# Optimization experiments

Hardware: AMD Instinct MI355X
Metric: run time of the kernel (lower is better)

## Reference

```python
import jax, jax.numpy as jnp
import numpy as np

S, B, E, H = 2048, 4, 512, 8
D = E // H

# --- Brevitas-style per-tensor fake quantization with straight-through estimator ---

def fq_s8(x):
    """Int8ActPerTensorFloat / Int8WeightPerTensorFloat: symmetric per-tensor abs-max."""
    qmax = 127.0
    scale = jnp.maximum(jnp.max(jnp.abs(x)), 1e-8) / qmax
    q = jnp.clip(jnp.round(x / scale), -128.0, qmax)
    return x + jax.lax.stop_gradient(scale * q - x), scale


def fq_u8(x):
    """Uint8ActPerTensorFloat for attention weights (softmax output, >=0)."""
    qmax = 255.0
    scale = jnp.maximum(jnp.max(x), 1e-8) / qmax
    q = jnp.clip(jnp.round(x / scale), 0.0, qmax)
    return x + jax.lax.stop_gradient(scale * q - x)


def fq_b32(b, scale):
    """Int32Bias: bias quantized with scale = input_scale * weight_scale."""
    qmax = 2.0 ** 31 - 1.0
    q = jnp.clip(jnp.round(b / scale), -qmax, qmax)
    return b + jax.lax.stop_gradient(scale * q - b)


def setup_inputs() -> dict:
    key = jax.random.key(0)
    ks = jax.random.split(key, 9)
    w = lambda k: jax.random.normal(k, (E, E), jnp.float32) * 0.02
    b = lambda k: jax.random.normal(k, (E,), jnp.float32) * 0.02
    return {
        "x": jax.random.normal(ks[0], (S, B, E), jnp.float32),
        "Wq": w(ks[1]), "Wk": w(ks[2]), "Wv": w(ks[3]),
        "bq": b(ks[4]), "bk": b(ks[5]), "bv": b(ks[6]),
        "Wo": w(ks[7]), "bo": b(ks[8]),
    }


def reference(x, Wq, Wk, Wv, bq, bk, bv, Wo, bo):
    # inputQuant (QuantIdentity, int8)
    xq, _ = fq_s8(x)
    # in_proj input quant (int8, per-tensor)
    xi, s_in = fq_s8(xq)

    def proj(W, b_):
        Wf, s_w = fq_s8(W)                    # int8 weight quant
        bf = fq_b32(b_, s_in * s_w)           # int32 bias quant
        return jnp.einsum('sbe,fe->sbf', xi, Wf) + bf

    q = proj(Wq, bq)  # [S,B,E]
    k = proj(Wk, bk)
    v = proj(Wv, bv)

    # split heads: [S,B,E] -> [B,H,S,D]
    heads = lambda t: t.reshape(S, B, H, D).transpose(1, 2, 0, 3)
    q, k, v = heads(q), heads(k), heads(v)

    qs, _ = fq_s8(q / jnp.sqrt(jnp.float32(D)))   # q_scaled_quant (int8)
    kt, _ = fq_s8(k)                              # k_transposed_quant (int8)
    scores = jnp.einsum('bhqd,bhkd->bhqk', qs, kt)  # [B,H,S,S]
    attn = fq_u8(jax.nn.softmax(scores, axis=-1))   # attn_output_weights_quant (uint8)
    vq, _ = fq_s8(v)                                # v_quant (int8)

    ctx = jnp.einsum('bhqk,bhkd->bhqd', attn, vq)   # [B,H,S,D]
    ctx = ctx.transpose(2, 0, 1, 3).reshape(S, B, E)  # back to [S,B,E]

    ci, s_c = fq_s8(ctx)                            # out_proj_input_quant
    Wof, s_wo = fq_s8(Wo)                           # out_proj_weight_quant
    bof = fq_b32(bo, s_c * s_wo)                    # out_proj_bias_quant
    y = jnp.einsum('sbe,fe->sbf', ci, Wof) + bof
    yq, _ = fq_s8(y)                                # out_proj_output_quant
    return yq
```

## Files before the change

### kernel.cpp

```cpp
#include <hip/hip_runtime.h>

constexpr int cS = 2048, cB = 4, cE = 512, cH = 8, cD = 64;
constexpr int cSB = cS * cB;
constexpr int cBH = cB * cH;
constexpr int cN  = cSB * cE;

typedef __bf16 v8bf  __attribute__((ext_vector_type(8)));
typedef float  f32x4 __attribute__((ext_vector_type(4)));

constexpr float cLOG2E = 1.4426950408889634f;


__device__ __forceinline__ unsigned short q2bf(float f) {
  return (unsigned short)(__float_as_uint(f) >> 16);
}
__device__ __forceinline__ float clip8(float t) { return fminf(fmaxf(t, -128.f), 127.f); }
__device__ __forceinline__ float wave_max(float v) {
#pragma unroll
  for (int o = 32; o > 0; o >>= 1) v = fmaxf(v, __shfl_down(v, o));
  return v;
}

__device__ __forceinline__ void stage8k(const unsigned short* __restrict__ gsrc,
                                        unsigned short* lds, int tid) {
  int w = tid >> 6;
#pragma unroll
  for (int is = 0; is < 2; ++is) {
    int c = is * 256 + tid;
    int cp = (c & ~7) | ((c & 7) ^ ((c >> 3) & 7));
    const char* g = (const char*)gsrc + (size_t)cp * 16;
    char* l = (char*)lds + (size_t)(is * 4096 + w * 1024);
    __builtin_amdgcn_global_load_lds(
        (const __attribute__((address_space(1))) unsigned int*)g,
        (__attribute__((address_space(3))) unsigned int*)l, 16, 0, 0);
  }
}
__device__ __forceinline__ v8bf lds_frag(const unsigned short* tile, int row, int chunk) {
  int sc = chunk ^ (row & 7);
  return *(const v8bf*)((const char*)tile + row * 128 + sc * 16);
}

__global__ void absmax_kernel(const float* __restrict__ p, int n4, unsigned* slot) {
  int tid = blockIdx.x * blockDim.x + threadIdx.x, stride = gridDim.x * blockDim.x;
  float m = 0.f;
  for (int i = tid; i < n4; i += stride) {
    float4 v = ((const float4*)p)[i];
    m = fmaxf(m, fmaxf(fmaxf(fabsf(v.x), fabsf(v.y)), fmaxf(fabsf(v.z), fabsf(v.w))));
  }
  m = wave_max(m);
  __shared__ float sm[4];
  int lane = threadIdx.x & 63, wid = threadIdx.x >> 6;
  if (lane == 0) sm[wid] = m;
  __syncthreads();
  if (threadIdx.x == 0) {
    float mm = sm[0];
    for (int w = 1; w < (int)blockDim.x / 64; ++w) mm = fmaxf(mm, sm[w]);
    atomicMax(slot, __float_as_uint(mm));
  }
}

__global__ void absmax4_kernel(const float* __restrict__ w0, const float* __restrict__ w1,
                               const float* __restrict__ w2, const float* __restrict__ w3,
                               int n4, unsigned* slots) {
  int y = blockIdx.y;
  const float* p = (y == 0) ? w0 : (y == 1) ? w1 : (y == 2) ? w2 : w3;
  int tid = blockIdx.x * blockDim.x + threadIdx.x, stride = gridDim.x * blockDim.x;
  float m = 0.f;
  for (int i = tid; i < n4; i += stride) {
    float4 v = ((const float4*)p)[i];
    m = fmaxf(m, fmaxf(fmaxf(fabsf(v.x), fabsf(v.y)), fmaxf(fabsf(v.z), fabsf(v.w))));
  }
  m = wave_max(m);
  __shared__ float sm[4];
  int lane = threadIdx.x & 63, wid = threadIdx.x >> 6;
  if (lane == 0) sm[wid] = m;
  __syncthreads();
  if (threadIdx.x == 0) {
    float mm = fmaxf(fmaxf(sm[0], sm[1]), fmaxf(sm[2], sm[3]));
    atomicMax(slots + y, __float_as_uint(mm));
  }
}

__global__ void scales_kernel(float* st, int stage) {
  if (stage == 0) {
    float s0 = fmaxf(st[0], 1e-8f) / 127.f;
    st[11] = s0;
    float mxq = s0 * 127.f;
    st[12] = fmaxf(mxq, 1e-8f) / 127.f;
    for (int i = 0; i < 4; ++i) st[13 + i] = fmaxf(st[1 + i], 1e-8f) / 127.f;
  } else if (stage == 1) {
    st[17] = fmaxf(st[5] * 0.125f, 1e-8f) / 127.f;
    st[18] = fmaxf(st[6], 1e-8f) / 127.f;
    st[19] = fmaxf(st[7], 1e-8f) / 127.f;
    st[25] = st[17] * st[18];
    st[26] = st[25] * cLOG2E;
  } else if (stage == 2) {
    float sa = fmaxf(st[8], 1e-8f) / 255.f;
    st[20] = sa; st[21] = 1.f / sa; st[22] = sa * st[19];
  } else if (stage == 3) {
    st[23] = fmaxf(st[9], 1e-8f) / 127.f;
  } else {
    st[24] = fmaxf(st[10], 1e-8f) / 127.f;
  }
}

__global__ void quant_x_kernel(const float* __restrict__ x, unsigned short* __restrict__ xq,
                               const float* st, int n4) {
  float s0 = st[11], si = st[12];
  int tid = blockIdx.x * blockDim.x + threadIdx.x, stride = gridDim.x * blockDim.x;
  for (int i = tid; i < n4; i += stride) {
    float4 v = ((const float4*)x)[i];
    ushort4 o; float t;
    t = s0 * clip8(rintf(v.x / s0)); o.x = q2bf(clip8(rintf(t / si)));
    t = s0 * clip8(rintf(v.y / s0)); o.y = q2bf(clip8(rintf(t / si)));
    t = s0 * clip8(rintf(v.z / s0)); o.z = q2bf(clip8(rintf(t / si)));
    t = s0 * clip8(rintf(v.w / s0)); o.w = q2bf(clip8(rintf(t / si)));
    ((ushort4*)xq)[i] = o;
  }
}

__global__ void quant_w4_kernel(const float* __restrict__ w0, const float* __restrict__ w1,
                                const float* __restrict__ w2, const float* __restrict__ w3,
                                unsigned short* __restrict__ outbase, int n4, const float* st) {
  int y = blockIdx.y;
  const float* in = (y == 0) ? w0 : (y == 1) ? w1 : (y == 2) ? w2 : w3;
  unsigned short* outp = outbase + (size_t)y * cE * cE;
  float s = st[13 + y];
  int tid = blockIdx.x * blockDim.x + threadIdx.x, stride = gridDim.x * blockDim.x;
  for (int i = tid; i < n4; i += stride) {
    float4 v = ((const float4*)in)[i];
    ushort4 o;
    o.x = q2bf(clip8(rintf(v.x / s)));
    o.y = q2bf(clip8(rintf(v.y / s)));
    o.z = q2bf(clip8(rintf(v.z / s)));
    o.w = q2bf(clip8(rintf(v.w / s)));
    ((ushort4*)outp)[i] = o;
  }
}

__global__ void quant_s8_kernel(const float* __restrict__ in, unsigned short* __restrict__ outp,
                                int n4, const float* st, int slot, float premul) {
  float s = st[slot];
  int tid = blockIdx.x * blockDim.x + threadIdx.x, stride = gridDim.x * blockDim.x;
  for (int i = tid; i < n4; i += stride) {
    float4 v = ((const float4*)in)[i];
    ushort4 o;
    o.x = q2bf(clip8(rintf(v.x * premul / s)));
    o.y = q2bf(clip8(rintf(v.y * premul / s)));
    o.z = q2bf(clip8(rintf(v.z * premul / s)));
    o.w = q2bf(clip8(rintf(v.w * premul / s)));
    ((ushort4*)outp)[i] = o;
  }
}

__global__ void quant_qk_kernel(const float* __restrict__ qf, unsigned short* __restrict__ qsb,
                                int n4, const float* st) {
  int y = blockIdx.y;
  const float* in = qf + (size_t)y * cN;
  unsigned short* outp = qsb + (size_t)y * cN;
  float s = st[17 + y];
  float premul = y ? 1.0f : 0.125f;
  int tid = blockIdx.x * blockDim.x + threadIdx.x, stride = gridDim.x * blockDim.x;
  for (int i = tid; i < n4; i += stride) {
    float4 v = ((const float4*)in)[i];
    ushort4 o;
    o.x = q2bf(clip8(rintf(v.x * premul / s)));
    o.y = q2bf(clip8(rintf(v.y * premul / s)));
    o.z = q2bf(clip8(rintf(v.z * premul / s)));
    o.w = q2bf(clip8(rintf(v.w * premul / s)));
    ((ushort4*)outp)[i] = o;
  }
}

__global__ void bias3_kernel(const float* __restrict__ b0, const float* __restrict__ b1,
                             const float* __restrict__ b2, float* __restrict__ bdst,
                             const float* st) {
  int y = blockIdx.y;
  const float* bsrc = (y == 0) ? b0 : (y == 1) ? b1 : b2;
  int f = blockIdx.x * blockDim.x + threadIdx.x;
  if (f < cE) {
    float s = st[12] * st[13 + y];
    bdst[y * cE + f] = s * rintf(bsrc[f] / s);
  }
}

__global__ void bias_kernel(const float* __restrict__ bsrc, float* __restrict__ bdst,
                            const float* st, int slot_in, int slot_w) {
  int f = blockIdx.x * blockDim.x + threadIdx.x;
  if (f < cE) {
    float s = st[slot_in] * st[slot_w];
    bdst[f] = s * rintf(bsrc[f] / s);
  }
}

__global__ __launch_bounds__(256) void quant_vT_kernel(const float* __restrict__ v,
                                                       unsigned short* __restrict__ vT,
                                                       const float* st) {
  __shared__ unsigned short tile[64][65];
  int bh = blockIdx.y, bx = blockIdx.x, s0 = bx * 64;
  float sv = st[19];
  int td = threadIdx.x & 63, tr = threadIdx.x >> 6;
  for (int r = tr; r < 64; r += 4)
    tile[r][td] = q2bf(clip8(rintf(v[((size_t)bh * cS + s0 + r) * cD + td] / sv)));
  __syncthreads();
  for (int r = tr; r < 64; r += 4)
    vT[((size_t)(bh * 32 + bx) * 64 + r) * 64 + td] = tile[td][r];
}

__global__ void final_quant_kernel(float* __restrict__ y, const float* st, int n4) {
  float s = st[24];
  int tid = blockIdx.x * blockDim.x + threadIdx.x, stride = gridDim.x * blockDim.x;
  for (int i = tid; i < n4; i += stride) {
    float4 v = ((float4*)y)[i];
    v.x = s * clip8(rintf(v.x / s)); v.y = s * clip8(rintf(v.y / s));
    v.z = s * clip8(rintf(v.z / s)); v.w = s * clip8(rintf(v.w / s));
    ((float4*)y)[i] = v;
  }
}

template <int OUTMODE>
__global__ __launch_bounds__(256) void gemm_kernel(const unsigned short* __restrict__ A,
                                                   const unsigned short* __restrict__ Wb,
                                                   const float* __restrict__ bias,
                                                   float* __restrict__ out, const float* st,
                                                   int slot_in, int slot_w, unsigned* amax_slot) {
  int wid = threadIdx.x >> 6, lane = threadIdx.x & 63;
  int wm = wid >> 1, wn = wid & 1;
  int row0 = blockIdx.x * 64 + wm * 32;
  int col0 = blockIdx.y * 64 + wn * 32;
  int lr = lane & 15, lk = (lane >> 4) * 8;
  f32x4 acc[2][2] = {};
  const unsigned short* a0p = A + (size_t)(row0 + lr) * cE + lk;
  const unsigned short* a1p = A + (size_t)(row0 + 16 + lr) * cE + lk;
  const unsigned short* b0p = Wb + (size_t)(col0 + lr) * cE + lk;
  const unsigned short* b1p = Wb + (size_t)(col0 + 16 + lr) * cE + lk;
  for (int e0 = 0; e0 < cE; e0 += 32) {
    v8bf a0 = *(const v8bf*)(a0p + e0), a1 = *(const v8bf*)(a1p + e0);
    v8bf b0 = *(const v8bf*)(b0p + e0), b1 = *(const v8bf*)(b1p + e0);
    acc[0][0] = __builtin_amdgcn_mfma_f32_16x16x32_bf16(a0, b0, acc[0][0], 0, 0, 0);
    acc[0][1] = __builtin_amdgcn_mfma_f32_16x16x32_bf16(a0, b1, acc[0][1], 0, 0, 0);
    acc[1][0] = __builtin_amdgcn_mfma_f32_16x16x32_bf16(a1, b0, acc[1][0], 0, 0, 0);
    acc[1][1] = __builtin_amdgcn_mfma_f32_16x16x32_bf16(a1, b1, acc[1][1], 0, 0, 0);
  }
  float scale = st[slot_in] * st[slot_w];
  float lmax = 0.f;
#pragma unroll
  for (int mi = 0; mi < 2; ++mi)
#pragma unroll
    for (int ni = 0; ni < 2; ++ni)
#pragma unroll
      for (int r = 0; r < 4; ++r) {
        int row = row0 + mi * 16 + (lane >> 4) * 4 + r;
        int col = col0 + ni * 16 + lr;
        float val = scale * acc[mi][ni][r] + bias[col];
        lmax = fmaxf(lmax, fabsf(val));
        if (OUTMODE == 0) {
          int s = row >> 2, bb = row & 3, h = col >> 6, d = col & 63;
          out[(((size_t)(bb * cH + h)) * cS + s) * cD + d] = val;
        } else {
          out[(size_t)row * cE + col] = val;
        }
      }
  lmax = wave_max(lmax);
  if (lane == 0) atomicMax(amax_slot, __float_as_uint(lmax));
}

__global__ __launch_bounds__(256) void attn_pass1_kernel(const unsigned short* __restrict__ qs,
                                                         const unsigned short* __restrict__ ks,
                                                         float* __restrict__ marr,
                                                         float* __restrict__ izarr,
                                                         const float* st, unsigned* maxiz_slot) {
  __shared__ __align__(16) unsigned short kbuf[2][64][64];
  int tid = threadIdx.x;
  int bh = blockIdx.y;
  int wid = tid >> 6, lane = tid & 63;
  int lr = lane & 15, g = lane >> 4, lk = g * 8;
  int r0 = blockIdx.x * 64 + wid * 16;
  float sscale2 = st[26];
  v8bf aq0 = *(const v8bf*)(qs + ((size_t)bh * cS + r0 + lr) * cD + lk);
  v8bf aq1 = *(const v8bf*)(qs + ((size_t)bh * cS + r0 + lr) * cD + 32 + lk);
  const unsigned short* Kb = ks + (size_t)bh * cS * cD;

  stage8k(Kb, &kbuf[0][0][0], tid);
  __syncthreads();
  float pm = -1e30f, zs = 0.f;
  int buf = 0;
  for (int t = 0; t < 32; ++t) {
    if (t < 31) stage8k(Kb + (size_t)(t + 1) * 4096, &kbuf[buf ^ 1][0][0], tid);
    const unsigned short* Kt = &kbuf[buf][0][0];
    f32x4 s4[4];
#pragma unroll
    for (int jc = 0; jc < 4; ++jc) {
      v8bf k0 = lds_frag(Kt, jc * 16 + lr, g);
      v8bf k1 = lds_frag(Kt, jc * 16 + lr, g + 4);
      f32x4 z = {0.f, 0.f, 0.f, 0.f};
      z = __builtin_amdgcn_mfma_f32_16x16x32_bf16(k0, aq0, z, 0, 0, 0);
      z = __builtin_amdgcn_mfma_f32_16x16x32_bf16(k1, aq1, z, 0, 0, 0);
      s4[jc] = z;
    }
    float tv[16];
#pragma unroll
    for (int jc = 0; jc < 4; ++jc)
#pragma unroll
      for (int r = 0; r < 4; ++r) tv[jc * 4 + r] = s4[jc][r] * sscale2;
    float tm = tv[0];
#pragma unroll
    for (int i = 1; i < 16; ++i) tm = fmaxf(tm, tv[i]);
    float nm = fmaxf(pm, tm);
    float acc = zs * __builtin_amdgcn_exp2f(pm - nm);
#pragma unroll
    for (int i = 0; i < 16; ++i) acc += __builtin_amdgcn_exp2f(tv[i] - nm);
    zs = acc; pm = nm;
    __syncthreads();
    buf ^= 1;
  }
#pragma unroll
  for (int o = 16; o < 64; o <<= 1) {
    float mo = __shfl_xor(pm, o);
    float zo = __shfl_xor(zs, o);
    float nm = fmaxf(pm, mo);
    zs = zs * __builtin_amdgcn_exp2f(pm - nm) + zo * __builtin_amdgcn_exp2f(mo - nm);
    pm = nm;
  }
  float iz = 1.0f / zs;
  if (g == 0) {
    marr[bh * cS + r0 + lr] = pm;
    izarr[bh * cS + r0 + lr] = iz;
  }
  float wmax = wave_max(iz);
  if (lane == 0) atomicMax(maxiz_slot, __float_as_uint(wmax));
}

__global__ __launch_bounds__(256) void attn_pass2_kernel(
    const unsigned short* __restrict__ qs, const unsigned short* __restrict__ ks,
    const unsigned short* __restrict__ vT, const float* __restrict__ marr,
    const float* __restrict__ izarr, float* __restrict__ ctx, const float* st,
    unsigned* amax_slot) {
  __shared__ __align__(16) unsigned short kbuf[2][64][64];
  __shared__ __align__(16) unsigned short vbuf[2][64][64];
  __shared__ __align__(16) unsigned short plds[4][16][88];
  int tid = threadIdx.x;
  int bh = blockIdx.y, b = bh >> 3, h = bh & 7;
  int wid = tid >> 6, lane = tid & 63;
  int lr = lane & 15, g = lane >> 4, lk = g * 8;
  int r0 = blockIdx.x * 64 + wid * 16;
  float sscale2 = st[26], isa = st[21], cscale = st[22];
  v8bf aq0 = *(const v8bf*)(qs + ((size_t)bh * cS + r0 + lr) * cD + lk);
  v8bf aq1 = *(const v8bf*)(qs + ((size_t)bh * cS + r0 + lr) * cD + 32 + lk);
  float m2 = marr[bh * cS + r0 + lr];
  float fac = izarr[bh * cS + r0 + lr] * isa;
  const unsigned short* Kb = ks + (size_t)bh * cS * cD;
  const unsigned short* Vb = vT + (size_t)bh * 32 * 4096;
  f32x4 cacc[4] = {};

  stage8k(Kb, &kbuf[0][0][0], tid);
  stage8k(Vb, &vbuf[0][0][0], tid);
  __syncthreads();
  int buf = 0;
  for (int t = 0; t < 32; ++t) {
    if (t < 31) {
      stage8k(Kb + (size_t)(t + 1) * 4096, &kbuf[buf ^ 1][0][0], tid);
      stage8k(Vb + (size_t)(t + 1) * 4096, &vbuf[buf ^ 1][0][0], tid);
    }
    const unsigned short* Kt = &kbuf[buf][0][0];
    const unsigned short* Vt = &vbuf[buf][0][0];
#pragma unroll
    for (int jc = 0; jc < 4; ++jc) {
      v8bf k0 = lds_frag(Kt, jc * 16 + lr, g);
      v8bf k1 = lds_frag(Kt, jc * 16 + lr, g + 4);
      f32x4 z = {0.f, 0.f, 0.f, 0.f};
      z = __builtin_amdgcn_mfma_f32_16x16x32_bf16(k0, aq0, z, 0, 0, 0);
      z = __builtin_amdgcn_mfma_f32_16x16x32_bf16(k1, aq1, z, 0, 0, 0);
      float a0 = fminf(rintf(__builtin_amdgcn_exp2f(__builtin_fmaf(z[0], sscale2, -m2)) * fac), 255.f);
      float a1 = fminf(rintf(__builtin_amdgcn_exp2f(__builtin_fmaf(z[1], sscale2, -m2)) * fac), 255.f);
      float a2 = fminf(rintf(__builtin_amdgcn_exp2f(__builtin_fmaf(z[2], sscale2, -m2)) * fac), 255.f);
      float a3 = fminf(rintf(__builtin_amdgcn_exp2f(__builtin_fmaf(z[3], sscale2, -m2)) * fac), 255.f);
      uint2 pw;
      pw.x = (__float_as_uint(a0) >> 16) | (__float_as_uint(a1) & 0xFFFF0000u);
      pw.y = (__float_as_uint(a2) >> 16) | (__float_as_uint(a3) & 0xFFFF0000u);
      *(uint2*)&plds[wid][lr][jc * 16 + g * 4] = pw;
    }
    v8bf ap0 = *(const v8bf*)&plds[wid][lr][lk];
    v8bf ap1 = *(const v8bf*)&plds[wid][lr][32 + lk];
#pragma unroll
    for (int dt = 0; dt < 4; ++dt) {
      v8bf v0 = lds_frag(Vt, dt * 16 + lr, g);
      v8bf v1 = lds_frag(Vt, dt * 16 + lr, g + 4);
      cacc[dt] = __builtin_amdgcn_mfma_f32_16x16x32_bf16(ap0, v0, cacc[dt], 0, 0, 0);
      cacc[dt] = __builtin_amdgcn_mfma_f32_16x16x32_bf16(ap1, v1, cacc[dt], 0, 0, 0);
    }
    __syncthreads();
    buf ^= 1;
  }
  float lmax = 0.f;
#pragma unroll
  for (int dt = 0; dt < 4; ++dt)
#pragma unroll
    for (int r = 0; r < 4; ++r) {
      int qrow = r0 + g * 4 + r;
      int d = dt * 16 + lr;
      float val = cscale * cacc[dt][r];
      lmax = fmaxf(lmax, fabsf(val));
      ctx[((size_t)qrow * cB + b) * cE + h * cD + d] = val;
    }
  lmax = wave_max(lmax);
  if (lane == 0) atomicMax(amax_slot, __float_as_uint(lmax));
}

extern "C" void kernel_launch(void* const* d_in, const int* in_sizes, int n_in, void* d_out,
                              int out_size, void* d_ws, size_t ws_size, hipStream_t stream) {
  (void)in_sizes; (void)n_in; (void)out_size; (void)ws_size;
  const float* x  = (const float*)d_in[0];
  const float* Wq = (const float*)d_in[1];
  const float* Wk = (const float*)d_in[2];
  const float* Wv = (const float*)d_in[3];
  const float* bq = (const float*)d_in[4];
  const float* bk = (const float*)d_in[5];
  const float* bv = (const float*)d_in[6];
  const float* Wo = (const float*)d_in[7];
  const float* bo = (const float*)d_in[8];
  float* out = (float*)d_out;

  char* ws = (char*)d_ws;
  size_t off = 0;
  auto alloc = [&](size_t bytes) { size_t o = off; off += (bytes + 255) & ~(size_t)255; return o; };
  float* st = (float*)(ws + alloc(64 * 4));
  unsigned short* xq  = (unsigned short*)(ws + alloc((size_t)cN * 2));
  unsigned short* wbq = (unsigned short*)(ws + alloc((size_t)cE * cE * 2));
  unsigned short* wbk = (unsigned short*)(ws + alloc((size_t)cE * cE * 2));
  unsigned short* wbv = (unsigned short*)(ws + alloc((size_t)cE * cE * 2));
  unsigned short* wbo = (unsigned short*)(ws + alloc((size_t)cE * cE * 2));
  float* bfq = (float*)(ws + alloc(cE * 4));
  float* bfk = (float*)(ws + alloc(cE * 4));
  float* bfv = (float*)(ws + alloc(cE * 4));
  float* bfo = (float*)(ws + alloc(cE * 4));
  float* qf = (float*)(ws + alloc((size_t)cN * 4));
  float* kf = (float*)(ws + alloc((size_t)cN * 4));
  float* vf = (float*)(ws + alloc((size_t)cN * 4));
  unsigned short* qsb = (unsigned short*)(ws + alloc((size_t)cN * 2));
  unsigned short* ksb = (unsigned short*)(ws + alloc((size_t)cN * 2));
  unsigned short* vTb = (unsigned short*)(ws + alloc((size_t)cN * 2));
  float* marr  = (float*)(ws + alloc((size_t)cBH * cS * 4));
  float* izarr = (float*)(ws + alloc((size_t)cBH * cS * 4));
  float* ctxf = qf;
  unsigned short* cib = (unsigned short*)kf;

  int n4 = cN / 4;
  int nw4 = cE * cE / 4;
  hipMemsetAsync(st, 0, 256, stream);
  absmax_kernel<<<1024, 256, 0, stream>>>(x, n4, (unsigned*)(st + 0));
  absmax4_kernel<<<dim3(64, 4), 256, 0, stream>>>(Wq, Wk, Wv, Wo, nw4, (unsigned*)(st + 1));
  scales_kernel<<<1, 1, 0, stream>>>(st, 0);
  quant_x_kernel<<<1024, 256, 0, stream>>>(x, xq, st, n4);
  quant_w4_kernel<<<dim3(64, 4), 256, 0, stream>>>(Wq, Wk, Wv, Wo, wbq, nw4, st);
  bias3_kernel<<<dim3(2, 3), 256, 0, stream>>>(bq, bk, bv, bfq, st);
  gemm_kernel<0><<<dim3(cSB / 64, cE / 64), 256, 0, stream>>>(xq, wbq, bfq, qf, st, 12, 13, (unsigned*)(st + 5));
  gemm_kernel<0><<<dim3(cSB / 64, cE / 64), 256, 0, stream>>>(xq, wbk, bfk, kf, st, 12, 14, (unsigned*)(st + 6));
  gemm_kernel<0><<<dim3(cSB / 64, cE / 64), 256, 0, stream>>>(xq, wbv, bfv, vf, st, 12, 15, (unsigned*)(st + 7));
  scales_kernel<<<1, 1, 0, stream>>>(st, 1);
  quant_qk_kernel<<<dim3(512, 2), 256, 0, stream>>>(qf, qsb, n4, st);
  quant_vT_kernel<<<dim3(cS / 64, cBH), 256, 0, stream>>>(vf, vTb, st);
  attn_pass1_kernel<<<dim3(cS / 64, cBH), 256, 0, stream>>>(qsb, ksb, marr, izarr, st, (unsigned*)(st + 8));
  scales_kernel<<<1, 1, 0, stream>>>(st, 2);
  attn_pass2_kernel<<<dim3(cS / 64, cBH), 256, 0, stream>>>(qsb, ksb, vTb, marr, izarr, ctxf, st, (unsigned*)(st + 9));
  scales_kernel<<<1, 1, 0, stream>>>(st, 3);
  quant_s8_kernel<<<1024, 256, 0, stream>>>(ctxf, cib, n4, st, 23, 1.0f);
  bias_kernel<<<2, 256, 0, stream>>>(bo, bfo, st, 23, 16);
  gemm_kernel<1><<<dim3(cSB / 64, cE / 64), 256, 0, stream>>>(cib, wbo, bfo, out, st, 23, 16, (unsigned*)(st + 10));
  scales_kernel<<<1, 1, 0, stream>>>(st, 4);
  final_quant_kernel<<<1024, 256, 0, stream>>>(out, st, n4);
}
```

Before: 574.5 us.

## Process 32 query rows per wave in attention passes to reuse K/V tiles

Both attention kernels now give each wave two 16-row query groups, so a block covers 128 query rows instead of 64 and the grid is halved. Every K and V fragment read from LDS and every staged tile feeds twice as many MFMAs. This cuts global and LDS traffic for K/V per query row. The cost is more registers per thread and a smaller grid of 512 blocks, which may lower occupancy and latency hiding.

```diff
diff --git a/kernel.cpp b/kernel.cpp
--- a/kernel.cpp
+++ b/kernel.cpp
@@ -275,59 +275,75 @@
   int bh = blockIdx.y;
   int wid = tid >> 6, lane = tid & 63;
   int lr = lane & 15, g = lane >> 4, lk = g * 8;
-  int r0 = blockIdx.x * 64 + wid * 16;
+  int r0 = blockIdx.x * 128 + wid * 32;
   float sscale2 = st[26];
-  v8bf aq0 = *(const v8bf*)(qs + ((size_t)bh * cS + r0 + lr) * cD + lk);
-  v8bf aq1 = *(const v8bf*)(qs + ((size_t)bh * cS + r0 + lr) * cD + 32 + lk);
+  v8bf aq0[2], aq1[2];
+#pragma unroll
+  for (int qg = 0; qg < 2; ++qg) {
+    const unsigned short* qp = qs + ((size_t)bh * cS + r0 + qg * 16 + lr) * cD + lk;
+    aq0[qg] = *(const v8bf*)qp; aq1[qg] = *(const v8bf*)(qp + 32);
+  }
   const unsigned short* Kb = ks + (size_t)bh * cS * cD;
 
   stage8k(Kb, &kbuf[0][0][0], tid);
   __syncthreads();
-  float pm = -1e30f, zs = 0.f;
+  float pm[2] = {-1e30f, -1e30f}, zs[2] = {0.f, 0.f};
   int buf = 0;
   for (int t = 0; t < 32; ++t) {
     if (t < 31) stage8k(Kb + (size_t)(t + 1) * 4096, &kbuf[buf ^ 1][0][0], tid);
     const unsigned short* Kt = &kbuf[buf][0][0];
-    f32x4 s4[4];
+    f32x4 s4[2][4];
 #pragma unroll
     for (int jc = 0; jc < 4; ++jc) {
       v8bf k0 = lds_frag(Kt, jc * 16 + lr, g);
       v8bf k1 = lds_frag(Kt, jc * 16 + lr, g + 4);
-      f32x4 z = {0.f, 0.f, 0.f, 0.f};
-      z = __builtin_amdgcn_mfma_f32_16x16x32_bf16(k0, aq0, z, 0, 0, 0);
-      z = __builtin_amdgcn_mfma_f32_16x16x32_bf16(k1, aq1, z, 0, 0, 0);
-      s4[jc] = z;
-    }
-    float tv[16];
-#pragma unroll
-    for (int jc = 0; jc < 4; ++jc)
-#pragma unroll
-      for (int r = 0; r < 4; ++r) tv[jc * 4 + r] = s4[jc][r] * sscale2;
-    float tm = tv[0];
-#pragma unroll
-    for (int i = 1; i < 16; ++i) tm = fmaxf(tm, tv[i]);
-    float nm = fmaxf(pm, tm);
-    float acc = zs * __builtin_amdgcn_exp2f(pm - nm);
-#pragma unroll
-    for (int i = 0; i < 16; ++i) acc += __builtin_amdgcn_exp2f(tv[i] - nm);
-    zs = acc; pm = nm;
+#pragma unroll
+      for (int qg = 0; qg < 2; ++qg) {
+        f32x4 z = {0.f, 0.f, 0.f, 0.f};
+        z = __builtin_amdgcn_mfma_f32_16x16x32_bf16(k0, aq0[qg], z, 0, 0, 0);
+        z = __builtin_amdgcn_mfma_f32_16x16x32_bf16(k1, aq1[qg], z, 0, 0, 0);
+        s4[qg][jc] = z;
+      }
+    }
+#pragma unroll
+    for (int qg = 0; qg < 2; ++qg) {
+      float tv[16];
+#pragma unroll
+      for (int jc = 0; jc < 4; ++jc)
+#pragma unroll
+        for (int r = 0; r < 4; ++r) tv[jc * 4 + r] = s4[qg][jc][r] * sscale2;
+      float tm = tv[0];
+#pragma unroll
+      for (int i = 1; i < 16; ++i) tm = fmaxf(tm, tv[i]);
+      float nm = fmaxf(pm[qg], tm);
+      float acc = zs[qg] * __builtin_amdgcn_exp2f(pm[qg] - nm);
+#pragma unroll
+      for (int i = 0; i < 16; ++i) acc += __builtin_amdgcn_exp2f(tv[i] - nm);
+      zs[qg] = acc; pm[qg] = nm;
+    }
     __syncthreads();
     buf ^= 1;
   }
-#pragma unroll
-  for (int o = 16; o < 64; o <<= 1) {
-    float mo = __shfl_xor(pm, o);
-    float zo = __shfl_xor(zs, o);
-    float nm = fmaxf(pm, mo);
-    zs = zs * __builtin_amdgcn_exp2f(pm - nm) + zo * __builtin_amdgcn_exp2f(mo - nm);
-    pm = nm;
-  }
-  float iz = 1.0f / zs;
-  if (g == 0) {
-    marr[bh * cS + r0 + lr] = pm;
-    izarr[bh * cS + r0 + lr] = iz;
-  }
-  float wmax = wave_max(iz);
+  float wm_l = 0.f;
+#pragma unroll
+  for (int qg = 0; qg < 2; ++qg) {
+    float m = pm[qg], z = zs[qg];
+#pragma unroll
+    for (int o = 16; o < 64; o <<= 1) {
+      float mo = __shfl_xor(m, o);
+      float zo = __shfl_xor(z, o);
+      float nm = fmaxf(m, mo);
+      z = z * __builtin_amdgcn_exp2f(m - nm) + zo * __builtin_amdgcn_exp2f(mo - nm);
+      m = nm;
+    }
+    float iz = 1.0f / z;
+    if (g == 0) {
+      marr[bh * cS + r0 + qg * 16 + lr] = m;
+      izarr[bh * cS + r0 + qg * 16 + lr] = iz;
+    }
+    wm_l = fmaxf(wm_l, iz);
+  }
+  float wmax = wave_max(wm_l);
   if (lane == 0) atomicMax(maxiz_slot, __float_as_uint(wmax));
 }
 
@@ -338,20 +354,25 @@
     unsigned* amax_slot) {
   __shared__ __align__(16) unsigned short kbuf[2][64][64];
   __shared__ __align__(16) unsigned short vbuf[2][64][64];
-  __shared__ __align__(16) unsigned short plds[4][16][88];
+  __shared__ __align__(16) unsigned short plds[4][2][16][88];
   int tid = threadIdx.x;
   int bh = blockIdx.y, b = bh >> 3, h = bh & 7;
   int wid = tid >> 6, lane = tid & 63;
   int lr = lane & 15, g = lane >> 4, lk = g * 8;
-  int r0 = blockIdx.x * 64 + wid * 16;
+  int r0 = blockIdx.x * 128 + wid * 32;
   float sscale2 = st[26], isa = st[21], cscale = st[22];
-  v8bf aq0 = *(const v8bf*)(qs + ((size_t)bh * cS + r0 + lr) * cD + lk);
-  v8bf aq1 = *(const v8bf*)(qs + ((size_t)bh * cS + r0 + lr) * cD + 32 + lk);
-  float m2 = marr[bh * cS + r0 + lr];
-  float fac = izarr[bh * cS + r0 + lr] * isa;
+  v8bf aq0[2], aq1[2];
+  float m2[2], fac[2];
+#pragma unroll
+  for (int qg = 0; qg < 2; ++qg) {
+    const unsigned short* qp = qs + ((size_t)bh * cS + r0 + qg * 16 + lr) * cD + lk;
+    aq0[qg] = *(const v8bf*)qp; aq1[qg] = *(const v8bf*)(qp + 32);
+    m2[qg] = marr[bh * cS + r0 + qg * 16 + lr];
+    fac[qg] = izarr[bh * cS + r0 + qg * 16 + lr] * isa;
+  }
   const unsigned short* Kb = ks + (size_t)bh * cS * cD;
   const unsigned short* Vb = vT + (size_t)bh * 32 * 4096;
-  f32x4 cacc[4] = {};
+  f32x4 cacc[2][4] = {};
 
   stage8k(Kb, &kbuf[0][0][0], tid);
   stage8k(Vb, &vbuf[0][0][0], tid);
@@ -368,41 +389,53 @@
     for (int jc = 0; jc < 4; ++jc) {
       v8bf k0 = lds_frag(Kt, jc * 16 + lr, g);
       v8bf k1 = lds_frag(Kt, jc * 16 + lr, g + 4);
-      f32x4 z = {0.f, 0.f, 0.f, 0.f};
-      z = __builtin_amdgcn_mfma_f32_16x16x32_bf16(k0, aq0, z, 0, 0, 0);
-      z = __builtin_amdgcn_mfma_f32_16x16x32_bf16(k1, aq1, z, 0, 0, 0);
-      float a0 = fminf(rintf(__builtin_amdgcn_exp2f(__builtin_fmaf(z[0], sscale2, -m2)) * fac), 255.f);
-      float a1 = fminf(rintf(__builtin_amdgcn_exp2f(__builtin_fmaf(z[1], sscale2, -m2)) * fac), 255.f);
-      float a2 = fminf(rintf(__builtin_amdgcn_exp2f(__builtin_fmaf(z[2], sscale2, -m2)) * fac), 255.f);
-      float a3 = fminf(rintf(__builtin_amdgcn_exp2f(__builtin_fmaf(z[3], sscale2, -m2)) * fac), 255.f);
-      uint2 pw;
-      pw.x = (__float_as_uint(a0) >> 16) | (__float_as_uint(a1) & 0xFFFF0000u);
-      pw.y = (__float_as_uint(a2) >> 16) | (__float_as_uint(a3) & 0xFFFF0000u);
-      *(uint2*)&plds[wid][lr][jc * 16 + g * 4] = pw;
-    }
-    v8bf ap0 = *(const v8bf*)&plds[wid][lr][lk];
-    v8bf ap1 = *(const v8bf*)&plds[wid][lr][32 + lk];
+#pragma unroll
+      for (int qg = 0; qg < 2; ++qg) {
+        f32x4 z = {0.f, 0.f, 0.f, 0.f};
+        z = __builtin_amdgcn_mfma_f32_16x16x32_bf16(k0, aq0[qg], z, 0, 0, 0);
+        z = __builtin_amdgcn_mfma_f32_16x16x32_bf16(k1, aq1[qg], z, 0, 0, 0);
+        float a0 = fminf(rintf(__builtin_amdgcn_exp2f(__builtin_fmaf(z[0], sscale2, -m2[qg])) * fac[qg]), 255.f);
+        float a1 = fminf(rintf(__builtin_amdgcn_exp2f(__builtin_fmaf(z[1], sscale2, -m2[qg])) * fac[qg]), 255.f);
+        float a2 = fminf(rintf(__builtin_amdgcn_exp2f(__builtin_fmaf(z[2], sscale2, -m2[qg])) * fac[qg]), 255.f);
+        float a3 = fminf(rintf(__builtin_amdgcn_exp2f(__builtin_fmaf(z[3], sscale2, -m2[qg])) * fac[qg]), 255.f);
+        uint2 pw;
+        pw.x = (__float_as_uint(a0) >> 16) | (__float_as_uint(a1) & 0xFFFF0000u);
+        pw.y = (__float_as_uint(a2) >> 16) | (__float_as_uint(a3) & 0xFFFF0000u);
+        *(uint2*)&plds[wid][qg][lr][jc * 16 + g * 4] = pw;
+      }
+    }
+    v8bf ap0[2], ap1[2];
+#pragma unroll
+    for (int qg = 0; qg < 2; ++qg) {
+      ap0[qg] = *(const v8bf*)&plds[wid][qg][lr][lk];
+      ap1[qg] = *(const v8bf*)&plds[wid][qg][lr][32 + lk];
+    }
 #pragma unroll
     for (int dt = 0; dt < 4; ++dt) {
       v8bf v0 = lds_frag(Vt, dt * 16 + lr, g);
       v8bf v1 = lds_frag(Vt, dt * 16 + lr, g + 4);
-      cacc[dt] = __builtin_amdgcn_mfma_f32_16x16x32_bf16(ap0, v0, cacc[dt], 0, 0, 0);
-      cacc[dt] = __builtin_amdgcn_mfma_f32_16x16x32_bf16(ap1, v1, cacc[dt], 0, 0, 0);
+#pragma unroll
+      for (int qg = 0; qg < 2; ++qg) {
+        cacc[qg][dt] = __builtin_amdgcn_mfma_f32_16x16x32_bf16(ap0[qg], v0, cacc[qg][dt], 0, 0, 0);
+        cacc[qg][dt] = __builtin_amdgcn_mfma_f32_16x16x32_bf16(ap1[qg], v1, cacc[qg][dt], 0, 0, 0);
+      }
     }
     __syncthreads();
     buf ^= 1;
   }
   float lmax = 0.f;
 #pragma unroll
-  for (int dt = 0; dt < 4; ++dt)
-#pragma unroll
-    for (int r = 0; r < 4; ++r) {
-      int qrow = r0 + g * 4 + r;
-      int d = dt * 16 + lr;
-      float val = cscale * cacc[dt][r];
-      lmax = fmaxf(lmax, fabsf(val));
-      ctx[((size_t)qrow * cB + b) * cE + h * cD + d] = val;
-    }
+  for (int qg = 0; qg < 2; ++qg)
+#pragma unroll
+    for (int dt = 0; dt < 4; ++dt)
+#pragma unroll
+      for (int r = 0; r < 4; ++r) {
+        int qrow = r0 + qg * 16 + g * 4 + r;
+        int d = dt * 16 + lr;
+        float val = cscale * cacc[qg][dt][r];
+        lmax = fmaxf(lmax, fabsf(val));
+        ctx[((size_t)qrow * cB + b) * cE + h * cD + d] = val;
+      }
   lmax = wave_max(lmax);
   if (lane == 0) atomicMax(amax_slot, __float_as_uint(lmax));
 }
@@ -460,9 +493,9 @@
   scales_kernel<<<1, 1, 0, stream>>>(st, 1);
   quant_qk_kernel<<<dim3(512, 2), 256, 0, stream>>>(qf, qsb, n4, st);
   quant_vT_kernel<<<dim3(cS / 64, cBH), 256, 0, stream>>>(vf, vTb, st);
-  attn_pass1_kernel<<<dim3(cS / 64, cBH), 256, 0, stream>>>(qsb, ksb, marr, izarr, st, (unsigned*)(st + 8));
+  attn_pass1_kernel<<<dim3(cS / 128, cBH), 256, 0, stream>>>(qsb, ksb, marr, izarr, st, (unsigned*)(st + 8));
   scales_kernel<<<1, 1, 0, stream>>>(st, 2);
-  attn_pass2_kernel<<<dim3(cS / 64, cBH), 256, 0, stream>>>(qsb, ksb, vTb, marr, izarr, ctxf, st, (unsigned*)(st + 9));
+  attn_pass2_kernel<<<dim3(cS / 128, cBH), 256, 0, stream>>>(qsb, ksb, vTb, marr, izarr, ctxf, st, (unsigned*)(st + 9));
   scales_kernel<<<1, 1, 0, stream>>>(st, 3);
   quant_s8_kernel<<<1024, 256, 0, stream>>>(ctxf, cib, n4, st, 23, 1.0f);
   bias_kernel<<<2, 256, 0, stream>>>(bo, bfo, st, 23, 16);
```

Result: faster. 535.0 us (-6.9%).
